# Performance work log

Measured on AMD Instinct MI355X. Metric: run time of the kernel, lower is better.

## Reference

```python
import jax, jax.numpy as jnp
import numpy as np

T = 0.1                    # softmax temperature
NEG = -65504.0             # torch.finfo(torch.float16).min, used by masked_fill_
EPS = 1e-12                # F.normalize eps


def setup_inputs() -> dict:
    key = jax.random.key(0)
    # (2*B, dim): two views stacked along batch, pre-normalization projector output
    features = jax.random.normal(key, (8192, 512), dtype=jnp.float32)
    return {"features": features}


def reference(features):
    # F.normalize(feats, dim=1)
    norm = jnp.maximum(jnp.linalg.norm(features, axis=1, keepdims=True), EPS)
    f = features / norm

    B = f.shape[0] // 2
    feat_a, feat_b = f[:B], f[B:]          # torch.chunk(features, 2)

    # world_size == 1 -> concat_all_gather is identity
    mask = jnp.eye(B, dtype=bool)

    logits_aa = jnp.where(mask, NEG, (feat_a @ feat_a.T) / T)   # [B, B]
    logits_bb = jnp.where(mask, NEG, (feat_b @ feat_b.T) / T)   # [B, B]
    logits_ab = (feat_a @ feat_b.T) / T                          # [B, B]
    logits_ba = (feat_b @ feat_a.T) / T                          # [B, B]

    tgt = jnp.arange(B)

    def ce(logits):
        # mean cross-entropy with targets = arange(B); positives sit in the
        # first (cross-view) block, i.e. column i of row i.
        logp = jax.nn.log_softmax(logits, axis=-1)   # [B, 2B]
        return -jnp.mean(logp[tgt, tgt])

    loss_a = ce(jnp.concatenate([logits_ab, logits_aa], axis=-1))
    loss_b = ce(jnp.concatenate([logits_ba, logits_bb], axis=-1))
    return loss_a + loss_b
```

## Files before the change

### kernel.cpp

```cpp
#include <hip/hip_runtime.h>
#include <hip/hip_bf16.h>

typedef __attribute__((ext_vector_type(4))) int i32x4;

#define NROW 8192
#define DIM 512
#define BHALF 4096
#define NB 64
#define BM 128
#define NPAIR 2080
#define XCHUNK 260

__device__ __forceinline__ void gload_lds16(const void* g, void* l) {
  __builtin_amdgcn_global_load_lds(
      (const __attribute__((address_space(1))) void*)g,
      (__attribute__((address_space(3))) void*)l,
      16, 0, 0);
}

template <int CTRL>
__device__ __forceinline__ float dpp_ror_add(float v) {
  const int r = __builtin_amdgcn_update_dpp(0, __float_as_int(v), CTRL, 0xf, 0xf, false);
  return v + __int_as_float(r);
}
__device__ __forceinline__ float sum16_dpp(float v) {
  v = dpp_ror_add<0x128>(v);
  v = dpp_ror_add<0x124>(v);
  v = dpp_ror_add<0x122>(v);
  v = dpp_ror_add<0x121>(v);
  return v;
}

__global__ __launch_bounds__(256) void normalize_kernel(const float* __restrict__ in,
                                                        signed char* __restrict__ out) {
  const int w = threadIdx.x >> 6, lane = threadIdx.x & 63;
  const int row = blockIdx.x * 4 + w;
  const float4* src = (const float4*)(in + (size_t)row * DIM) + lane * 2;
  const float4 v0 = src[0], v1 = src[1];
  float ss = v0.x * v0.x + v0.y * v0.y + v0.z * v0.z + v0.w * v0.w
           + v1.x * v1.x + v1.y * v1.y + v1.z * v1.z + v1.w * v1.w;
  #pragma unroll
  for (int m = 1; m < 64; m <<= 1) ss += __shfl_xor(ss, m);
  const float s127 = 127.0f / fmaxf(sqrtf(ss), 1e-12f);
  float vv[8] = {v0.x, v0.y, v0.z, v0.w, v1.x, v1.y, v1.z, v1.w};
  signed char q[8];
  #pragma unroll
  for (int j = 0; j < 8; ++j) {
    int qi = __float2int_rn(vv[j] * s127);
    qi = qi > 127 ? 127 : (qi < -127 ? -127 : qi);
    q[j] = (signed char)qi;
  }
  *(int2*)(out + (size_t)row * 512 + lane * 8) = *(const int2*)q;
}

__global__ __launch_bounds__(256, 4) void pair_gram_kernel(const signed char* __restrict__ f8,
                                                           float* __restrict__ psum,
                                                           float* __restrict__ ppos) {
  __shared__ __align__(16) char lds[32768];

  const int bid = blockIdx.x;
  const int wg = (bid & 7) * XCHUNK + (bid >> 3);
  int rem = wg, MI = 0, MJ = 0;
  {
    bool brk = false;
    for (MI = 0; MI < 4 && !brk; ++MI) {
      for (MJ = MI; MJ < 4; ++MJ) {
        const int sz = (MI == MJ) ? 136 : 256;
        if (rem < sz) { brk = true; break; }
        rem -= sz;
      }
    }
    if (brk) --MI;
  }
  int ib, jb;
  if (MI == MJ) {
    int i = 0, b = 0;
    while (b + (16 - i) <= rem) { b += 16 - i; ++i; }
    ib = MI * 16 + i; jb = MI * 16 + i + (rem - b);
  } else {
    ib = MI * 16 + (rem >> 4); jb = MJ * 16 + (rem & 15);
  }
  const bool has_pos = (jb == ib + 32);

  const int tid = threadIdx.x;
  const int lane = tid & 63;
  const int w = tid >> 6;
  const int wy = w >> 1;
  const int wx = w & 1;
  const int fr = lane & 15;
  const int g = lane >> 4;

  const int srow8 = lane >> 3;
  const int scol = (lane & 7) ^ srow8;
  const signed char* gA = f8 + (size_t)(ib * BM + w * 8 + srow8) * 512 + scol * 16;
  const signed char* gB = f8 + (size_t)(jb * BM + w * 8 + srow8) * 512 + scol * 16;
  char* dA = lds + w * 1024;
  char* dB = lds + 16384 + w * 1024;

  i32x4 acc[4][4];
  const i32x4 izero = {0, 0, 0, 0};
  #pragma unroll
  for (int mi = 0; mi < 4; ++mi)
    #pragma unroll
    for (int ni = 0; ni < 4; ++ni) acc[mi][ni] = izero;

  const int f7 = fr & 7;
  const int sk0 = ((0 + g) ^ f7) * 16;
  const int sk1 = ((4 + g) ^ f7) * 16;
  const int arow = (wy * 64 + fr) * 128;
  const int brow = 16384 + (wx * 64 + fr) * 128;

  for (int t = 0; t < 4; ++t) {
    __syncthreads();
    const int k0 = t * 128;
    #pragma unroll
    for (int q = 0; q < 4; ++q) {
      gload_lds16(gA + k0 + (size_t)q * 32 * 512, dA + q * 4096);
      gload_lds16(gB + k0 + (size_t)q * 32 * 512, dB + q * 4096);
    }
    __syncthreads();

    #pragma unroll
    for (int ks = 0; ks < 2; ++ks) {
      const int sk = ks ? sk1 : sk0;
      i32x4 aF[4], bF[4];
      #pragma unroll
      for (int mi = 0; mi < 4; ++mi) aF[mi] = *(const i32x4*)(lds + arow + mi * 2048 + sk);
      #pragma unroll
      for (int ni = 0; ni < 4; ++ni) bF[ni] = *(const i32x4*)(lds + brow + ni * 2048 + sk);
      __builtin_amdgcn_s_setprio(1);
      #pragma unroll
      for (int mi = 0; mi < 4; ++mi)
        #pragma unroll
        for (int ni = 0; ni < 4; ++ni)
          acc[mi][ni] = __builtin_amdgcn_mfma_i32_16x16x64_i8(aF[mi], bF[ni], acc[mi][ni], 0, 0, 0);
      __builtin_amdgcn_s_setprio(0);
    }
  }

  const float SC10 = 10.0f / 16129.0f;
  const bool isdiag = (ib == jb);
  float rsum[4][4], csum[4];
  #pragma unroll
  for (int mi = 0; mi < 4; ++mi)
    #pragma unroll
    for (int r = 0; r < 4; ++r) rsum[mi][r] = 0.f;
  #pragma unroll
  for (int ni = 0; ni < 4; ++ni) csum[ni] = 0.f;

  #pragma unroll
  for (int mi = 0; mi < 4; ++mi) {
    #pragma unroll
    for (int ni = 0; ni < 4; ++ni) {
      const int lc = wx * 64 + ni * 16 + fr;
      #pragma unroll
      for (int r = 0; r < 4; ++r) {
        const int lr = wy * 64 + mi * 16 + g * 4 + r;
        const float l10 = (float)acc[mi][ni][r] * SC10;
        const float e = (isdiag && lc == lr) ? 0.f : __expf(l10 - 10.0f);
        rsum[mi][r] += e;
        csum[ni] += e;
      }
    }
  }

  #pragma unroll
  for (int mi = 0; mi < 4; ++mi)
    #pragma unroll
    for (int r = 0; r < 4; ++r) rsum[mi][r] = sum16_dpp(rsum[mi][r]);
  #pragma unroll
  for (int ni = 0; ni < 4; ++ni) {
    float a = csum[ni];
    a += __shfl_xor(a, 16);
    a += __shfl_xor(a, 32);
    csum[ni] = a;
  }

  __syncthreads();
  float* sc = (float*)lds;
  if (fr == 0) {
    #pragma unroll
    for (int mi = 0; mi < 4; ++mi)
      #pragma unroll
      for (int r = 0; r < 4; ++r) {
        const int row = wy * 64 + mi * 16 + g * 4 + r;
        sc[wx * 128 + row] = rsum[mi][r];
      }
  }
  if (g == 0) {
    #pragma unroll
    for (int ni = 0; ni < 4; ++ni) {
      const int col = wx * 64 + ni * 16 + fr;
      sc[256 + wy * 128 + col] = csum[ni];
    }
  }
  if (has_pos && wy == wx) {
    #pragma unroll
    for (int mi = 0; mi < 4; ++mi)
      #pragma unroll
      for (int r = 0; r < 4; ++r)
        if (fr == g * 4 + r) {
          const int lr = wy * 64 + mi * 16 + g * 4 + r;
          sc[512 + lr] = (float)acc[mi][mi][r] * (1.0f / 16129.0f);
        }
  }
  __syncthreads();

  if (tid < 128) {
    const int row = tid;
    const float s = sc[row] + sc[128 + row];
    const float p = has_pos ? sc[512 + row] : 0.f;
    psum[(size_t)jb * NROW + ib * BM + row] = s;
    ppos[(size_t)jb * NROW + ib * BM + row] = p;
  } else if (ib != jb) {
    const int col = tid - 128;
    const float s = sc[256 + col] + sc[384 + col];
    const float p = has_pos ? sc[512 + col] : 0.f;
    psum[(size_t)ib * NROW + jb * BM + col] = s;
    ppos[(size_t)ib * NROW + jb * BM + col] = p;
  }
}

__global__ __launch_bounds__(128) void loss_stage1(const float* __restrict__ psum,
                                                   const float* __restrict__ ppos,
                                                   float* __restrict__ partial) {
  const int row = blockIdx.x * 128 + threadIdx.x;
  float s = 0.f, p = 0.f;
  #pragma unroll 8
  for (int sl = 0; sl < NB; ++sl) {
    s += psum[(size_t)sl * NROW + row];
    p += ppos[(size_t)sl * NROW + row];
  }
  float local = logf(s) + 10.0f - 10.0f * p;
  #pragma unroll
  for (int m = 1; m < 64; m <<= 1) local += __shfl_xor(local, m);
  __shared__ float red[2];
  if ((threadIdx.x & 63) == 0) red[threadIdx.x >> 6] = local;
  __syncthreads();
  if (threadIdx.x == 0) partial[blockIdx.x] = red[0] + red[1];
}

__global__ __launch_bounds__(64) void loss_stage2(const float* __restrict__ partial,
                                                  float* __restrict__ out) {
  float v = partial[threadIdx.x];
  #pragma unroll
  for (int m = 1; m < 64; m <<= 1) v += __shfl_xor(v, m);
  if (threadIdx.x == 0) out[0] = v * (1.0f / (float)BHALF);
}

extern "C" void kernel_launch(void* const* d_in, const int* in_sizes, int n_in,
                              void* d_out, int out_size, void* d_ws, size_t ws_size,
                              hipStream_t stream) {
  const float* feat = (const float*)d_in[0];
  char* ws = (char*)d_ws;
  signed char* f8 = (signed char*)ws;
  float* psum = (float*)(ws + (size_t)NROW * 512);
  float* ppos = psum + (size_t)NB * NROW;
  float* partial = ppos + (size_t)NB * NROW;
  float* out = (float*)d_out;

  normalize_kernel<<<NROW / 4, 256, 0, stream>>>(feat, f8);
  pair_gram_kernel<<<NPAIR, 256, 0, stream>>>(f8, psum, ppos);
  loss_stage1<<<NROW / 128, 128, 0, stream>>>(psum, ppos, partial);
  loss_stage2<<<1, 64, 0, stream>>>(partial, out);
}
```

Baseline: 46.87 us.

## Use two-wave 128x64 warp tiles and drop the dense positive-logit buffer

The pair-gram kernel moves from four waves with 64x64 tiles each to two waves, each computing a 128x64 tile (8x4 MFMA fragments). This raises A-fragment reuse per wave and halves the block's thread count. The dense ppos partial array is replaced by a compact per-row positive array written directly from registers, so stage1 no longer reads 64 slices of positives. In exchange, each wave holds twice the accumulators and registers, which lowers occupancy, and each block now has only two waves to hide latency.

```diff
diff --git a/kernel.cpp b/kernel.cpp
--- a/kernel.cpp
+++ b/kernel.cpp
@@ -53,9 +53,9 @@
   *(int2*)(out + (size_t)row * 512 + lane * 8) = *(const int2*)q;
 }
 
-__global__ __launch_bounds__(256, 4) void pair_gram_kernel(const signed char* __restrict__ f8,
+__global__ __launch_bounds__(128, 2) void pair_gram_kernel(const signed char* __restrict__ f8,
                                                            float* __restrict__ psum,
-                                                           float* __restrict__ ppos) {
+                                                           float* __restrict__ posArr) {
   __shared__ __align__(16) char lds[32768];
 
   const int bid = blockIdx.x;
@@ -81,56 +81,55 @@
     ib = MI * 16 + (rem >> 4); jb = MJ * 16 + (rem & 15);
   }
   const bool has_pos = (jb == ib + 32);
+  const bool isdiag = (ib == jb);
 
   const int tid = threadIdx.x;
   const int lane = tid & 63;
   const int w = tid >> 6;
-  const int wy = w >> 1;
-  const int wx = w & 1;
   const int fr = lane & 15;
   const int g = lane >> 4;
 
-  const int srow8 = lane >> 3;
-  const int scol = (lane & 7) ^ srow8;
-  const signed char* gA = f8 + (size_t)(ib * BM + w * 8 + srow8) * 512 + scol * 16;
-  const signed char* gB = f8 + (size_t)(jb * BM + w * 8 + srow8) * 512 + scol * 16;
+  const int srow = tid >> 3;
+  const int scol = (tid & 7) ^ (srow & 7);
+  const signed char* gA = f8 + (size_t)(ib * BM + srow) * 512 + scol * 16;
+  const signed char* gB = f8 + (size_t)(jb * BM + srow) * 512 + scol * 16;
   char* dA = lds + w * 1024;
   char* dB = lds + 16384 + w * 1024;
 
-  i32x4 acc[4][4];
+  i32x4 acc[8][4];
   const i32x4 izero = {0, 0, 0, 0};
   #pragma unroll
-  for (int mi = 0; mi < 4; ++mi)
+  for (int mi = 0; mi < 8; ++mi)
     #pragma unroll
     for (int ni = 0; ni < 4; ++ni) acc[mi][ni] = izero;
 
   const int f7 = fr & 7;
   const int sk0 = ((0 + g) ^ f7) * 16;
   const int sk1 = ((4 + g) ^ f7) * 16;
-  const int arow = (wy * 64 + fr) * 128;
-  const int brow = 16384 + (wx * 64 + fr) * 128;
+  const int arow = fr * 128;
+  const int brow = 16384 + (w * 64 + fr) * 128;
 
   for (int t = 0; t < 4; ++t) {
     __syncthreads();
     const int k0 = t * 128;
     #pragma unroll
-    for (int q = 0; q < 4; ++q) {
-      gload_lds16(gA + k0 + (size_t)q * 32 * 512, dA + q * 4096);
-      gload_lds16(gB + k0 + (size_t)q * 32 * 512, dB + q * 4096);
+    for (int q = 0; q < 8; ++q) {
+      gload_lds16(gA + k0 + (size_t)q * 16 * 512, dA + q * 2048);
+      gload_lds16(gB + k0 + (size_t)q * 16 * 512, dB + q * 2048);
     }
     __syncthreads();
 
     #pragma unroll
     for (int ks = 0; ks < 2; ++ks) {
       const int sk = ks ? sk1 : sk0;
-      i32x4 aF[4], bF[4];
-      #pragma unroll
-      for (int mi = 0; mi < 4; ++mi) aF[mi] = *(const i32x4*)(lds + arow + mi * 2048 + sk);
+      i32x4 aF[8], bF[4];
+      #pragma unroll
+      for (int mi = 0; mi < 8; ++mi) aF[mi] = *(const i32x4*)(lds + arow + mi * 2048 + sk);
       #pragma unroll
       for (int ni = 0; ni < 4; ++ni) bF[ni] = *(const i32x4*)(lds + brow + ni * 2048 + sk);
       __builtin_amdgcn_s_setprio(1);
       #pragma unroll
-      for (int mi = 0; mi < 4; ++mi)
+      for (int mi = 0; mi < 8; ++mi)
         #pragma unroll
         for (int ni = 0; ni < 4; ++ni)
           acc[mi][ni] = __builtin_amdgcn_mfma_i32_16x16x64_i8(aF[mi], bF[ni], acc[mi][ni], 0, 0, 0);
@@ -139,33 +138,37 @@
   }
 
   const float SC10 = 10.0f / 16129.0f;
-  const bool isdiag = (ib == jb);
-  float rsum[4][4], csum[4];
-  #pragma unroll
-  for (int mi = 0; mi < 4; ++mi)
+  float rsum[8][4], csum[4];
+  #pragma unroll
+  for (int mi = 0; mi < 8; ++mi)
     #pragma unroll
     for (int r = 0; r < 4; ++r) rsum[mi][r] = 0.f;
   #pragma unroll
   for (int ni = 0; ni < 4; ++ni) csum[ni] = 0.f;
 
   #pragma unroll
-  for (int mi = 0; mi < 4; ++mi) {
+  for (int mi = 0; mi < 8; ++mi) {
     #pragma unroll
     for (int ni = 0; ni < 4; ++ni) {
-      const int lc = wx * 64 + ni * 16 + fr;
+      const int lc = w * 64 + ni * 16 + fr;
       #pragma unroll
       for (int r = 0; r < 4; ++r) {
-        const int lr = wy * 64 + mi * 16 + g * 4 + r;
+        const int lr = mi * 16 + g * 4 + r;
         const float l10 = (float)acc[mi][ni][r] * SC10;
         const float e = (isdiag && lc == lr) ? 0.f : __expf(l10 - 10.0f);
         rsum[mi][r] += e;
         csum[ni] += e;
+        if (has_pos && lc == lr) {
+          const float d = (float)acc[mi][ni][r] * (1.0f / 16129.0f);
+          posArr[ib * BM + lr] = d;
+          posArr[jb * BM + lr] = d;
+        }
       }
     }
   }
 
   #pragma unroll
-  for (int mi = 0; mi < 4; ++mi)
+  for (int mi = 0; mi < 8; ++mi)
     #pragma unroll
     for (int r = 0; r < 4; ++r) rsum[mi][r] = sum16_dpp(rsum[mi][r]);
   #pragma unroll
@@ -180,58 +183,35 @@
   float* sc = (float*)lds;
   if (fr == 0) {
     #pragma unroll
-    for (int mi = 0; mi < 4; ++mi)
-      #pragma unroll
-      for (int r = 0; r < 4; ++r) {
-        const int row = wy * 64 + mi * 16 + g * 4 + r;
-        sc[wx * 128 + row] = rsum[mi][r];
-      }
+    for (int mi = 0; mi < 8; ++mi)
+      #pragma unroll
+      for (int r = 0; r < 4; ++r)
+        sc[w * 128 + mi * 16 + g * 4 + r] = rsum[mi][r];
   }
   if (g == 0) {
     #pragma unroll
-    for (int ni = 0; ni < 4; ++ni) {
-      const int col = wx * 64 + ni * 16 + fr;
-      sc[256 + wy * 128 + col] = csum[ni];
-    }
-  }
-  if (has_pos && wy == wx) {
-    #pragma unroll
-    for (int mi = 0; mi < 4; ++mi)
-      #pragma unroll
-      for (int r = 0; r < 4; ++r)
-        if (fr == g * 4 + r) {
-          const int lr = wy * 64 + mi * 16 + g * 4 + r;
-          sc[512 + lr] = (float)acc[mi][mi][r] * (1.0f / 16129.0f);
-        }
+    for (int ni = 0; ni < 4; ++ni)
+      sc[256 + w * 64 + ni * 16 + fr] = csum[ni];
   }
   __syncthreads();
 
-  if (tid < 128) {
+  {
     const int row = tid;
     const float s = sc[row] + sc[128 + row];
-    const float p = has_pos ? sc[512 + row] : 0.f;
     psum[(size_t)jb * NROW + ib * BM + row] = s;
-    ppos[(size_t)jb * NROW + ib * BM + row] = p;
-  } else if (ib != jb) {
-    const int col = tid - 128;
-    const float s = sc[256 + col] + sc[384 + col];
-    const float p = has_pos ? sc[512 + col] : 0.f;
-    psum[(size_t)ib * NROW + jb * BM + col] = s;
-    ppos[(size_t)ib * NROW + jb * BM + col] = p;
+    if (!isdiag)
+      psum[(size_t)ib * NROW + jb * BM + row] = sc[256 + row];
   }
 }
 
 __global__ __launch_bounds__(128) void loss_stage1(const float* __restrict__ psum,
-                                                   const float* __restrict__ ppos,
+                                                   const float* __restrict__ posArr,
                                                    float* __restrict__ partial) {
   const int row = blockIdx.x * 128 + threadIdx.x;
-  float s = 0.f, p = 0.f;
+  float s = 0.f;
   #pragma unroll 8
-  for (int sl = 0; sl < NB; ++sl) {
-    s += psum[(size_t)sl * NROW + row];
-    p += ppos[(size_t)sl * NROW + row];
-  }
-  float local = logf(s) + 10.0f - 10.0f * p;
+  for (int sl = 0; sl < NB; ++sl) s += psum[(size_t)sl * NROW + row];
+  float local = logf(s) + 10.0f - 10.0f * posArr[row];
   #pragma unroll
   for (int m = 1; m < 64; m <<= 1) local += __shfl_xor(local, m);
   __shared__ float red[2];
@@ -255,12 +235,12 @@
   char* ws = (char*)d_ws;
   signed char* f8 = (signed char*)ws;
   float* psum = (float*)(ws + (size_t)NROW * 512);
-  float* ppos = psum + (size_t)NB * NROW;
-  float* partial = ppos + (size_t)NB * NROW;
+  float* posArr = psum + (size_t)NB * NROW;
+  float* partial = posArr + NROW;
   float* out = (float*)d_out;
 
   normalize_kernel<<<NROW / 4, 256, 0, stream>>>(feat, f8);
-  pair_gram_kernel<<<NPAIR, 256, 0, stream>>>(f8, psum, ppos);
-  loss_stage1<<<NROW / 128, 128, 0, stream>>>(psum, ppos, partial);
+  pair_gram_kernel<<<NPAIR, 128, 0, stream>>>(f8, psum, posArr);
+  loss_stage1<<<NROW / 128, 128, 0, stream>>>(psum, posArr, partial);
   loss_stage2<<<1, 64, 0, stream>>>(partial, out);
 }
```

Result: no change. 47.01 us (+0.3%).

## Double-buffer LDS K-tiles in int8 gram kernel and compact positive storage

Applied to the files above, without the earlier changes.

The gram kernel's K loop changes from four 128-wide stages with two barriers each to eight 64-wide stages, double-buffered in LDS. The next tile's global-to-LDS load is issued before the MFMAs on the current tile, and the swizzle is adjusted to match. The per-pair positive array (64×8192 floats) is replaced by a single 8192-entry array that only the positive-pair blocks write directly. This cuts write and read traffic in loss_stage1 and removes one LDS staging step. The cost is a single vmcnt(0)+barrier per smaller step and more loop iterations.

```diff
diff --git a/kernel.cpp b/kernel.cpp
--- a/kernel.cpp
+++ b/kernel.cpp
@@ -55,7 +55,7 @@
 
 __global__ __launch_bounds__(256, 4) void pair_gram_kernel(const signed char* __restrict__ f8,
                                                            float* __restrict__ psum,
-                                                           float* __restrict__ ppos) {
+                                                           float* __restrict__ posArr) {
   __shared__ __align__(16) char lds[32768];
 
   const int bid = blockIdx.x;
@@ -81,6 +81,7 @@
     ib = MI * 16 + (rem >> 4); jb = MJ * 16 + (rem & 15);
   }
   const bool has_pos = (jb == ib + 32);
+  const bool isdiag = (ib == jb);
 
   const int tid = threadIdx.x;
   const int lane = tid & 63;
@@ -90,12 +91,10 @@
   const int fr = lane & 15;
   const int g = lane >> 4;
 
-  const int srow8 = lane >> 3;
-  const int scol = (lane & 7) ^ srow8;
-  const signed char* gA = f8 + (size_t)(ib * BM + w * 8 + srow8) * 512 + scol * 16;
-  const signed char* gB = f8 + (size_t)(jb * BM + w * 8 + srow8) * 512 + scol * 16;
-  char* dA = lds + w * 1024;
-  char* dB = lds + 16384 + w * 1024;
+  const int srow4 = lane >> 2;
+  const int schunk = (lane & 3) ^ ((lane >> 3) & 3);
+  const signed char* gA = f8 + (size_t)(ib * BM + w * 32 + srow4) * 512 + schunk * 16;
+  const signed char* gB = f8 + (size_t)(jb * BM + w * 32 + srow4) * 512 + schunk * 16;
 
   i32x4 acc[4][4];
   const i32x4 izero = {0, 0, 0, 0};
@@ -104,42 +103,44 @@
     #pragma unroll
     for (int ni = 0; ni < 4; ++ni) acc[mi][ni] = izero;
 
-  const int f7 = fr & 7;
-  const int sk0 = ((0 + g) ^ f7) * 16;
-  const int sk1 = ((4 + g) ^ f7) * 16;
-  const int arow = (wy * 64 + fr) * 128;
-  const int brow = 16384 + (wx * 64 + fr) * 128;
-
-  for (int t = 0; t < 4; ++t) {
-    __syncthreads();
-    const int k0 = t * 128;
-    #pragma unroll
-    for (int q = 0; q < 4; ++q) {
-      gload_lds16(gA + k0 + (size_t)q * 32 * 512, dA + q * 4096);
-      gload_lds16(gB + k0 + (size_t)q * 32 * 512, dB + q * 4096);
-    }
-    __syncthreads();
-
-    #pragma unroll
-    for (int ks = 0; ks < 2; ++ks) {
-      const int sk = ks ? sk1 : sk0;
-      i32x4 aF[4], bF[4];
+  const int sk = (g ^ ((fr >> 1) & 3)) * 16;
+  const int arow = (wy * 64 + fr) * 64 + sk;
+  const int brow = 8192 + (wx * 64 + fr) * 64 + sk;
+
+  #define STAGE(buf, kt)                                                        \
+    {                                                                           \
+      char* _d = lds + (buf) * 16384 + w * 2048;                                \
+      const int _kn = (kt) * 64;                                                \
+      _Pragma("unroll")                                                         \
+      for (int q = 0; q < 2; ++q) {                                             \
+        gload_lds16(gA + _kn + (size_t)(q * 16) * 512, _d + q * 1024);          \
+        gload_lds16(gB + _kn + (size_t)(q * 16) * 512, _d + 8192 + q * 1024);   \
+      }                                                                         \
+    }
+
+  STAGE(0, 0);
+
+  for (int t = 0; t < 8; ++t) {
+    asm volatile("s_waitcnt vmcnt(0)\n\ts_barrier" ::: "memory");
+    if (t < 7) STAGE((t + 1) & 1, t + 1);
+
+    const char* base = lds + (t & 1) * 16384;
+    i32x4 aF[4], bF[4];
+    #pragma unroll
+    for (int mi = 0; mi < 4; ++mi) aF[mi] = *(const i32x4*)(base + arow + mi * 1024);
+    #pragma unroll
+    for (int ni = 0; ni < 4; ++ni) bF[ni] = *(const i32x4*)(base + brow + ni * 1024);
+    __builtin_amdgcn_s_setprio(1);
+    #pragma unroll
+    for (int mi = 0; mi < 4; ++mi)
       #pragma unroll
-      for (int mi = 0; mi < 4; ++mi) aF[mi] = *(const i32x4*)(lds + arow + mi * 2048 + sk);
-      #pragma unroll
-      for (int ni = 0; ni < 4; ++ni) bF[ni] = *(const i32x4*)(lds + brow + ni * 2048 + sk);
-      __builtin_amdgcn_s_setprio(1);
-      #pragma unroll
-      for (int mi = 0; mi < 4; ++mi)
-        #pragma unroll
-        for (int ni = 0; ni < 4; ++ni)
-          acc[mi][ni] = __builtin_amdgcn_mfma_i32_16x16x64_i8(aF[mi], bF[ni], acc[mi][ni], 0, 0, 0);
-      __builtin_amdgcn_s_setprio(0);
-    }
-  }
+      for (int ni = 0; ni < 4; ++ni)
+        acc[mi][ni] = __builtin_amdgcn_mfma_i32_16x16x64_i8(aF[mi], bF[ni], acc[mi][ni], 0, 0, 0);
+    __builtin_amdgcn_s_setprio(0);
+  }
+  #undef STAGE
 
   const float SC10 = 10.0f / 16129.0f;
-  const bool isdiag = (ib == jb);
   float rsum[4][4], csum[4];
   #pragma unroll
   for (int mi = 0; mi < 4; ++mi)
@@ -160,6 +161,11 @@
         const float e = (isdiag && lc == lr) ? 0.f : __expf(l10 - 10.0f);
         rsum[mi][r] += e;
         csum[ni] += e;
+        if (has_pos && lc == lr) {
+          const float d = (float)acc[mi][ni][r] * (1.0f / 16129.0f);
+          posArr[ib * BM + lr] = d;
+          posArr[jb * BM + lr] = d;
+        }
       }
     }
   }
@@ -194,44 +200,25 @@
       sc[256 + wy * 128 + col] = csum[ni];
     }
   }
-  if (has_pos && wy == wx) {
-    #pragma unroll
-    for (int mi = 0; mi < 4; ++mi)
-      #pragma unroll
-      for (int r = 0; r < 4; ++r)
-        if (fr == g * 4 + r) {
-          const int lr = wy * 64 + mi * 16 + g * 4 + r;
-          sc[512 + lr] = (float)acc[mi][mi][r] * (1.0f / 16129.0f);
-        }
-  }
   __syncthreads();
 
   if (tid < 128) {
     const int row = tid;
-    const float s = sc[row] + sc[128 + row];
-    const float p = has_pos ? sc[512 + row] : 0.f;
-    psum[(size_t)jb * NROW + ib * BM + row] = s;
-    ppos[(size_t)jb * NROW + ib * BM + row] = p;
-  } else if (ib != jb) {
+    psum[(size_t)jb * NROW + ib * BM + row] = sc[row] + sc[128 + row];
+  } else if (!isdiag) {
     const int col = tid - 128;
-    const float s = sc[256 + col] + sc[384 + col];
-    const float p = has_pos ? sc[512 + col] : 0.f;
-    psum[(size_t)ib * NROW + jb * BM + col] = s;
-    ppos[(size_t)ib * NROW + jb * BM + col] = p;
+    psum[(size_t)ib * NROW + jb * BM + col] = sc[256 + col] + sc[384 + col];
   }
 }
 
 __global__ __launch_bounds__(128) void loss_stage1(const float* __restrict__ psum,
-                                                   const float* __restrict__ ppos,
+                                                   const float* __restrict__ posArr,
                                                    float* __restrict__ partial) {
   const int row = blockIdx.x * 128 + threadIdx.x;
-  float s = 0.f, p = 0.f;
+  float s = 0.f;
   #pragma unroll 8
-  for (int sl = 0; sl < NB; ++sl) {
-    s += psum[(size_t)sl * NROW + row];
-    p += ppos[(size_t)sl * NROW + row];
-  }
-  float local = logf(s) + 10.0f - 10.0f * p;
+  for (int sl = 0; sl < NB; ++sl) s += psum[(size_t)sl * NROW + row];
+  float local = logf(s) + 10.0f - 10.0f * posArr[row];
   #pragma unroll
   for (int m = 1; m < 64; m <<= 1) local += __shfl_xor(local, m);
   __shared__ float red[2];
@@ -255,12 +242,12 @@
   char* ws = (char*)d_ws;
   signed char* f8 = (signed char*)ws;
   float* psum = (float*)(ws + (size_t)NROW * 512);
-  float* ppos = psum + (size_t)NB * NROW;
-  float* partial = ppos + (size_t)NB * NROW;
+  float* posArr = psum + (size_t)NB * NROW;
+  float* partial = posArr + NROW;
   float* out = (float*)d_out;
 
   normalize_kernel<<<NROW / 4, 256, 0, stream>>>(feat, f8);
-  pair_gram_kernel<<<NPAIR, 256, 0, stream>>>(f8, psum, ppos);
-  loss_stage1<<<NROW / 128, 128, 0, stream>>>(psum, ppos, partial);
+  pair_gram_kernel<<<NPAIR, 256, 0, stream>>>(f8, psum, posArr);
+  loss_stage1<<<NROW / 128, 128, 0, stream>>>(psum, posArr, partial);
   loss_stage2<<<1, 64, 0, stream>>>(partial, out);
 }
```

Result: faster. 45.32 us (-3.3%).
